# Optimization experiments

Hardware: AMD Instinct MI355X
Metric: run time of the kernel (lower is better)

Reference implementation:

```python
import jax, jax.numpy as jnp
import numpy as np

QI8_MIN, QI8_MAX = -128.0, 127.0   # torch.qint8 iinfo
QU8_MIN, QU8_MAX = 0.0, 255.0      # torch.quint8 iinfo


def _assym_scale_offset(v, qmin, qmax):
    # mirrors get_tensor_assym_scale_offset: scale=(max-min)/(qmax-qmin), offset=qmin - min/scale
    vmin = v.min()
    vmax = v.max()
    scale = (vmax - vmin) / (qmax - qmin)
    offset = qmin - vmin / scale
    return scale, offset


def _fake_quant(v, scale, zp, qmin, qmax):
    # torch.quantize_per_tensor: q = clamp(round(v/scale + zp), qmin, qmax); dequant = (q - zp)*scale
    q = jnp.clip(jnp.round(v / scale + zp), qmin, qmax)
    return (q - zp) * scale


def setup_inputs() -> dict:
    key = jax.random.key(0)
    k1, k2, k3 = jax.random.split(key, 3)
    x = jax.random.normal(k1, (8192, 4096), jnp.float32)          # quantized activation input (modeled as float)
    weight = jax.random.normal(k2, (4096, 4096), jnp.float32) * 0.02  # Linear.weight [out, in]
    bias = jax.random.normal(k3, (4096,), jnp.float32) * 0.01
    return {"x": x, "weight": weight, "bias": bias}


def reference(x, weight, bias):
    # --- weight quantization (qint8, per-tensor asymmetric, done at __init__) ---
    w_scale, w_off = _assym_scale_offset(weight, QI8_MIN, QI8_MAX)
    w_zp = jnp.round(w_off)  # torch casts zero_point to int
    w_dq = _fake_quant(weight, w_scale, w_zp, QI8_MIN, QI8_MAX)

    # --- input is a quint8 quantized tensor; model quantize->dequantize ---
    x_scale, x_off = _assym_scale_offset(x, QU8_MIN, QU8_MAX)
    x_zp = jnp.round(x_off)
    x_dq = _fake_quant(x, x_scale, x_zp, QU8_MIN, QU8_MAX)

    # --- calibration pass (not _computed): float Linear on dequantized input ---
    act = x_dq @ weight.T + bias                 # [tokens, out]
    a_scale, a_off = _assym_scale_offset(act, QU8_MIN, QU8_MAX)
    a_zp = jnp.round(a_off)

    # --- qF.linear: int8 GEMM (dequantized form) + bias, requantized to quint8 ---
    out = x_dq @ w_dq.T + bias
    return _fake_quant(out, a_scale, a_zp, QU8_MIN, QU8_MAX)
```

## Files before the change

kernel.cpp:

```cpp
#include <hip/hip_runtime.h>
#include <stdint.h>

#define M_DIM 8192
#define N_DIM 4096
#define K_DIM 4096

typedef __attribute__((ext_vector_type(4))) int i32x4;

__device__ __forceinline__ unsigned fkey(float f) {
  unsigned u = __float_as_uint(f);
  return (u & 0x80000000u) ? ~u : (u | 0x80000000u);
}
__device__ __forceinline__ float finv(unsigned k) {
  return __uint_as_float((k & 0x80000000u) ? (k ^ 0x80000000u) : ~k);
}
__device__ __forceinline__ void async16(const void* g, void* l) {
  __builtin_amdgcn_global_load_lds(
      (const __attribute__((address_space(1))) void*)g,
      (__attribute__((address_space(3))) void*)l, 16, 0, 0);
}

__global__ void minmax_fused(const float* __restrict__ x, const float* __restrict__ w,
                             unsigned* __restrict__ stats) {
  const bool isX = blockIdx.x < 2048;
  const float4* v4 = isX ? (const float4*)x : (const float4*)w;
  const int n4 = isX ? (M_DIM * K_DIM / 4) : (N_DIM * K_DIM / 4);
  const int bid = isX ? blockIdx.x : (blockIdx.x - 2048);
  const int nb = isX ? 2048 : 1024;
  int i0 = bid * blockDim.x + threadIdx.x;
  int stride = nb * blockDim.x;
  float vmin = 3.4e38f, vmax = -3.4e38f;
  for (int i = i0; i < n4; i += stride) {
    float4 t = v4[i];
    vmin = fminf(vmin, fminf(fminf(t.x, t.y), fminf(t.z, t.w)));
    vmax = fmaxf(vmax, fmaxf(fmaxf(t.x, t.y), fmaxf(t.z, t.w)));
  }
  unsigned kmin = fkey(vmin), kmax = ~fkey(vmax);
  #pragma unroll
  for (int off = 32; off; off >>= 1) {
    unsigned t0 = __shfl_down(kmin, (unsigned)off, 64);
    unsigned t1 = __shfl_down(kmax, (unsigned)off, 64);
    kmin = kmin < t0 ? kmin : t0;
    kmax = kmax < t1 ? kmax : t1;
  }
  if ((threadIdx.x & 63) == 0) {
    int base = isX ? 0 : 2;
    atomicMin(&stats[base + 0], kmin);
    atomicMin(&stats[base + 1], kmax);
  }
}

__global__ void quant_fused(const float* __restrict__ x, const float* __restrict__ w,
                            const unsigned* __restrict__ stats,
                            signed char* __restrict__ A8, signed char* __restrict__ B8,
                            signed char* __restrict__ R8,
                            int* __restrict__ rowA, int* __restrict__ colB, int* __restrict__ colR) {
  __shared__ int sr[8];
  const int tid = threadIdx.x;
  const int lane = tid & 63;
  const int wv = tid >> 6;
  if (blockIdx.x < M_DIM) {
    const int row = blockIdx.x;
    const float xmin = finv(stats[0]), xmax = finv(~stats[1]);
    const float xs = (xmax - xmin) / 255.0f;
    const float xzp = rintf(0.0f - xmin / xs);
    const float4* xr = (const float4*)(x + (size_t)row * K_DIM);
    char4* ar = (char4*)(A8 + (size_t)row * K_DIM);
    int s = 0;
    #pragma unroll
    for (int i = 0; i < 4; ++i) {
      int idx = tid + i * 256;
      float4 t = xr[idx];
      int q0 = (int)(fminf(fmaxf(rintf(t.x / xs + xzp), 0.f), 255.f)) - 128;
      int q1 = (int)(fminf(fmaxf(rintf(t.y / xs + xzp), 0.f), 255.f)) - 128;
      int q2 = (int)(fminf(fmaxf(rintf(t.z / xs + xzp), 0.f), 255.f)) - 128;
      int q3 = (int)(fminf(fmaxf(rintf(t.w / xs + xzp), 0.f), 255.f)) - 128;
      char4 c4; c4.x = (signed char)q0; c4.y = (signed char)q1;
      c4.z = (signed char)q2; c4.w = (signed char)q3;
      ar[idx] = c4;
      s += q0 + q1 + q2 + q3;
    }
    #pragma unroll
    for (int off = 32; off; off >>= 1) s += __shfl_down(s, (unsigned)off, 64);
    if (lane == 0) sr[wv] = s;
    __syncthreads();
    if (tid == 0) rowA[row] = sr[0] + sr[1] + sr[2] + sr[3];
  } else {
    const int row = blockIdx.x - M_DIM;
    const float wmin = finv(stats[2]), wmax = finv(~stats[3]);
    const float ws = (wmax - wmin) / 255.0f;
    const float wzp = rintf(-128.0f - wmin / ws);
    const float inv_rs = 126.0f / ws;
    const float4* wr = (const float4*)(w + (size_t)row * K_DIM);
    char4* br = (char4*)(B8 + (size_t)row * K_DIM);
    char4* rr = (char4*)(R8 + (size_t)row * K_DIM);
    int sb = 0, srr = 0;
    #pragma unroll
    for (int i = 0; i < 4; ++i) {
      int idx = tid + i * 256;
      float4 t = wr[idx];
      char4 bq, rq;
      float v, qf; int q, r;
      v = t.x; qf = fminf(fmaxf(rintf(v / ws + wzp), -128.f), 127.f); q = (int)qf;
      r = (int)fminf(fmaxf(rintf((v - ws * (qf - wzp)) * inv_rs), -127.f), 127.f);
      bq.x = (signed char)q; rq.x = (signed char)r; sb += q; srr += r;
      v = t.y; qf = fminf(fmaxf(rintf(v / ws + wzp), -128.f), 127.f); q = (int)qf;
      r = (int)fminf(fmaxf(rintf((v - ws * (qf - wzp)) * inv_rs), -127.f), 127.f);
      bq.y = (signed char)q; rq.y = (signed char)r; sb += q; srr += r;
      v = t.z; qf = fminf(fmaxf(rintf(v / ws + wzp), -128.f), 127.f); q = (int)qf;
      r = (int)fminf(fmaxf(rintf((v - ws * (qf - wzp)) * inv_rs), -127.f), 127.f);
      bq.z = (signed char)q; rq.z = (signed char)r; sb += q; srr += r;
      v = t.w; qf = fminf(fmaxf(rintf(v / ws + wzp), -128.f), 127.f); q = (int)qf;
      r = (int)fminf(fmaxf(rintf((v - ws * (qf - wzp)) * inv_rs), -127.f), 127.f);
      bq.w = (signed char)q; rq.w = (signed char)r; sb += q; srr += r;
      br[idx] = bq; rr[idx] = rq;
    }
    #pragma unroll
    for (int off = 32; off; off >>= 1) {
      sb += __shfl_down(sb, (unsigned)off, 64);
      srr += __shfl_down(srr, (unsigned)off, 64);
    }
    if (lane == 0) { sr[wv] = sb; sr[4 + wv] = srr; }
    __syncthreads();
    if (tid == 0) {
      colB[row] = sr[0] + sr[1] + sr[2] + sr[3];
      colR[row] = sr[4] + sr[5] + sr[6] + sr[7];
    }
  }
}

__global__ __launch_bounds__(512, 4) void gemm_i8(
    const signed char* __restrict__ A8, const signed char* __restrict__ B8,
    const signed char* __restrict__ R8,
    const int* __restrict__ rowA, const int* __restrict__ colB, const int* __restrict__ colR,
    const float* __restrict__ bias, unsigned* __restrict__ stats,
    float* __restrict__ outp) {
  __shared__ __align__(16) signed char sA[2 * 128 * 64];
  __shared__ __align__(16) signed char sB[2 * 128 * 64];
  __shared__ __align__(16) signed char sR[2 * 128 * 64];
  __shared__ unsigned s_red[2];

  const int tid = threadIdx.x;
  const int wave = tid >> 6;
  const int lane = tid & 63;
  const int xcd = blockIdx.x & 7;
  const int s = blockIdx.x >> 3;
  const int bn = xcd * 4 + (s >> 6);
  const int bm = s & 63;
  const int rowBase = bm * 128;
  const int colBase = bn * 128;
  const int wr = wave >> 2;
  const int wc = wave & 3;
  const int laneR = lane & 15;
  const int laneK = (lane >> 4) * 16;

  if (tid == 0) { s_red[0] = 0xFFFFFFFFu; s_red[1] = 0xFFFFFFFFu; }

  i32x4 acc_q[4][2];
  i32x4 acc_r[4][2];
  const i32x4 zero = {0, 0, 0, 0};
  #pragma unroll
  for (int i = 0; i < 4; ++i) { acc_q[i][0] = zero; acc_q[i][1] = zero;
                                acc_r[i][0] = zero; acc_r[i][1] = zero; }

  const signed char* srcA = A8 + (size_t)(rowBase + wave * 16 + laneR) * K_DIM + laneK;
  const signed char* srcB = B8 + (size_t)(colBase + wave * 16 + laneR) * K_DIM + laneK;
  const signed char* srcR = R8 + (size_t)(colBase + wave * 16 + laneR) * K_DIM + laneK;
  signed char* dA = sA + wave * 1024 + lane * 16;
  signed char* dB = sB + wave * 1024 + lane * 16;
  signed char* dR = sR + wave * 1024 + lane * 16;

#define STAGE(b, kt) do {                        \
    async16(srcA + (kt), dA + (b) * 8192);       \
    async16(srcB + (kt), dB + (b) * 8192);       \
    async16(srcR + (kt), dR + (b) * 8192);       \
  } while (0)

#define COMPUTE(b) do {                                                        \
    i32x4 af[4];                                                               \
    _Pragma("unroll")                                                          \
    for (int mi = 0; mi < 4; ++mi)                                             \
      af[mi] = *(const i32x4*)(sA + (b) * 8192 + (wr * 4 + mi) * 1024 + lane * 16); \
    _Pragma("unroll")                                                          \
    for (int ni = 0; ni < 2; ++ni) {                                           \
      const int bo = (b) * 8192 + (wc * 2 + ni) * 1024 + lane * 16;            \
      i32x4 bf = *(const i32x4*)(sB + bo);                                     \
      i32x4 rf = *(const i32x4*)(sR + bo);                                     \
      _Pragma("unroll")                                                        \
      for (int mi = 0; mi < 4; ++mi) {                                         \
        acc_q[mi][ni] = __builtin_amdgcn_mfma_i32_16x16x64_i8(af[mi], bf, acc_q[mi][ni], 0, 0, 0); \
        acc_r[mi][ni] = __builtin_amdgcn_mfma_i32_16x16x64_i8(af[mi], rf, acc_r[mi][ni], 0, 0, 0); \
      }                                                                        \
    }                                                                          \
  } while (0)

  STAGE(0, 0);
  __syncthreads();

  for (int kt = 0; kt < K_DIM - 128; kt += 128) {
    STAGE(1, kt + 64);
    COMPUTE(0);
    __syncthreads();
    STAGE(0, kt + 128);
    COMPUTE(1);
    __syncthreads();
  }
  STAGE(1, K_DIM - 64);
  COMPUTE(0);
  __syncthreads();
  COMPUTE(1);

#undef STAGE
#undef COMPUTE

  const float xmin = finv(stats[0]), xmax = finv(~stats[1]);
  const float xs = (xmax - xmin) / 255.0f;
  const float xzp = rintf(0.0f - xmin / xs);
  const float wmin = finv(stats[2]), wmax = finv(~stats[3]);
  const float ws = (wmax - wmin) / 255.0f;
  const float wzp = rintf(-128.0f - wmin / ws);
  const int c = 128 - (int)xzp;
  const int wzpi = (int)wzp;
  const float sw = xs * ws;
  const float xrs = xs * (ws / 126.0f);
  const int ccK = c * wzpi * K_DIM;
  unsigned kmin = 0xFFFFFFFFu, kmax = 0xFFFFFFFFu;

  int rAv[4][4];
  #pragma unroll
  for (int mi = 0; mi < 4; ++mi) {
    const int row0 = rowBase + wr * 64 + mi * 16 + (lane >> 4) * 4;
    #pragma unroll
    for (int r = 0; r < 4; ++r) rAv[mi][r] = rowA[row0 + r];
  }

  #pragma unroll
  for (int ni = 0; ni < 2; ++ni) {
    const int col = colBase + wc * 32 + ni * 16 + laneR;
    const float bv = bias[col];
    const int base_n = c * colB[col] - ccK;
    const int cR = c * colR[col];
    #pragma unroll
    for (int mi = 0; mi < 4; ++mi) {
      const int row0 = rowBase + wr * 64 + mi * 16 + (lane >> 4) * 4;
      #pragma unroll
      for (int r = 0; r < 4; ++r) {
        const int S = acc_q[mi][ni][r] + base_n - wzpi * rAv[mi][r];
        const float ov = sw * (float)S + bv;
        const int S2 = acc_r[mi][ni][r] + cR;
        const float av = ov + xrs * (float)S2;
        const unsigned k = fkey(av);
        const unsigned kf = ~k;
        kmin = kmin < k ? kmin : k;
        kmax = kmax < kf ? kmax : kf;
        outp[(size_t)(row0 + r) * N_DIM + col] = ov;
      }
    }
  }

  #pragma unroll
  for (int off = 32; off; off >>= 1) {
    unsigned t0 = __shfl_down(kmin, (unsigned)off, 64);
    unsigned t1 = __shfl_down(kmax, (unsigned)off, 64);
    kmin = kmin < t0 ? kmin : t0;
    kmax = kmax < t1 ? kmax : t1;
  }
  __syncthreads();
  if (lane == 0) { atomicMin(&s_red[0], kmin); atomicMin(&s_red[1], kmax); }
  __syncthreads();
  if (tid == 0) { atomicMin(&stats[4], s_red[0]); atomicMin(&stats[5], s_red[1]); }
}

__global__ void requant_kernel(float* __restrict__ out, const unsigned* __restrict__ stats, int n4) {
  const float amin = finv(stats[4]), amax = finv(~stats[5]);
  const float as = (amax - amin) / 255.0f;
  const float azp = rintf(0.0f - amin / as);
  float4* o4 = (float4*)out;
  int i0 = blockIdx.x * blockDim.x + threadIdx.x;
  int stride = gridDim.x * blockDim.x;
  for (int i = i0; i < n4; i += stride) {
    float4 t = o4[i];
    t.x = (fminf(fmaxf(rintf(t.x / as + azp), 0.f), 255.f) - azp) * as;
    t.y = (fminf(fmaxf(rintf(t.y / as + azp), 0.f), 255.f) - azp) * as;
    t.z = (fminf(fmaxf(rintf(t.z / as + azp), 0.f), 255.f) - azp) * as;
    t.w = (fminf(fmaxf(rintf(t.w / as + azp), 0.f), 255.f) - azp) * as;
    o4[i] = t;
  }
}

extern "C" void kernel_launch(void* const* d_in, const int* in_sizes, int n_in,
                              void* d_out, int out_size, void* d_ws, size_t ws_size,
                              hipStream_t stream) {
  const float* x = (const float*)d_in[0];
  const float* w = (const float*)d_in[1];
  const float* bias = (const float*)d_in[2];
  float* out = (float*)d_out;

  unsigned* stats = (unsigned*)d_ws;
  signed char* A8 = (signed char*)d_ws + 256;
  signed char* B8 = A8 + (size_t)M_DIM * K_DIM;
  signed char* R8 = B8 + (size_t)N_DIM * K_DIM;
  int* rowA = (int*)(R8 + (size_t)N_DIM * K_DIM);
  int* colB = rowA + M_DIM;
  int* colR = colB + N_DIM;

  hipMemsetAsync(stats, 0xFF, 24, stream);
  minmax_fused<<<3072, 256, 0, stream>>>(x, w, stats);
  quant_fused<<<M_DIM + N_DIM, 256, 0, stream>>>(x, w, stats, A8, B8, R8, rowA, colB, colR);
  gemm_i8<<<(M_DIM / 128) * (N_DIM / 128), 512, 0, stream>>>(A8, B8, R8, rowA, colB, colR, bias, stats, out);
  requant_kernel<<<2048, 256, 0, stream>>>(out, stats, M_DIM * N_DIM / 4);
}
```

Baseline: 980.6 us.

## Triple-buffer int8 GEMM LDS staging with vmcnt-gated barriers and MFMA priority

Moves the int8 GEMM main loop from double to triple LDS buffering with rotating offsets. Each step waits with a partial vmcnt instead of a full __syncthreads, so one 64-wide k-tile load stays in flight while the block computes. It also preloads B/R fragments before the MFMA block and raises wave priority around the MFMAs. LDS use per block grows from 48KB to 72KB, which may cut occupancy below the 4 blocks per CU targeted by the launch bounds.

```diff
diff --git a/kernel.cpp b/kernel.cpp
--- a/kernel.cpp
+++ b/kernel.cpp
@@ -135,9 +135,9 @@
     const int* __restrict__ rowA, const int* __restrict__ colB, const int* __restrict__ colR,
     const float* __restrict__ bias, unsigned* __restrict__ stats,
     float* __restrict__ outp) {
-  __shared__ __align__(16) signed char sA[2 * 128 * 64];
-  __shared__ __align__(16) signed char sB[2 * 128 * 64];
-  __shared__ __align__(16) signed char sR[2 * 128 * 64];
+  __shared__ __align__(16) signed char sA[3 * 128 * 64];
+  __shared__ __align__(16) signed char sB[3 * 128 * 64];
+  __shared__ __align__(16) signed char sR[3 * 128 * 64];
   __shared__ unsigned s_red[2];
 
   const int tid = threadIdx.x;
@@ -170,45 +170,55 @@
   signed char* dB = sB + wave * 1024 + lane * 16;
   signed char* dR = sR + wave * 1024 + lane * 16;
 
-#define STAGE(b, kt) do {                        \
-    async16(srcA + (kt), dA + (b) * 8192);       \
-    async16(srcB + (kt), dB + (b) * 8192);       \
-    async16(srcR + (kt), dR + (b) * 8192);       \
+#define STAGE(off, kt) do {                      \
+    async16(srcA + (kt), dA + (off));            \
+    async16(srcB + (kt), dB + (off));            \
+    async16(srcR + (kt), dR + (off));            \
   } while (0)
 
-#define COMPUTE(b) do {                                                        \
+#define COMPUTE(off) do {                                                      \
     i32x4 af[4];                                                               \
     _Pragma("unroll")                                                          \
     for (int mi = 0; mi < 4; ++mi)                                             \
-      af[mi] = *(const i32x4*)(sA + (b) * 8192 + (wr * 4 + mi) * 1024 + lane * 16); \
+      af[mi] = *(const i32x4*)(sA + (off) + (wr * 4 + mi) * 1024 + lane * 16); \
+    i32x4 bf[2], rf[2];                                                        \
     _Pragma("unroll")                                                          \
     for (int ni = 0; ni < 2; ++ni) {                                           \
-      const int bo = (b) * 8192 + (wc * 2 + ni) * 1024 + lane * 16;            \
-      i32x4 bf = *(const i32x4*)(sB + bo);                                     \
-      i32x4 rf = *(const i32x4*)(sR + bo);                                     \
+      const int bo = (off) + (wc * 2 + ni) * 1024 + lane * 16;                 \
+      bf[ni] = *(const i32x4*)(sB + bo);                                       \
+      rf[ni] = *(const i32x4*)(sR + bo);                                       \
+    }                                                                          \
+    __builtin_amdgcn_s_setprio(1);                                             \
+    _Pragma("unroll")                                                          \
+    for (int ni = 0; ni < 2; ++ni) {                                           \
       _Pragma("unroll")                                                        \
       for (int mi = 0; mi < 4; ++mi) {                                         \
-        acc_q[mi][ni] = __builtin_amdgcn_mfma_i32_16x16x64_i8(af[mi], bf, acc_q[mi][ni], 0, 0, 0); \
-        acc_r[mi][ni] = __builtin_amdgcn_mfma_i32_16x16x64_i8(af[mi], rf, acc_r[mi][ni], 0, 0, 0); \
+        acc_q[mi][ni] = __builtin_amdgcn_mfma_i32_16x16x64_i8(af[mi], bf[ni], acc_q[mi][ni], 0, 0, 0); \
+        acc_r[mi][ni] = __builtin_amdgcn_mfma_i32_16x16x64_i8(af[mi], rf[ni], acc_r[mi][ni], 0, 0, 0); \
       }                                                                        \
     }                                                                          \
+    __builtin_amdgcn_s_setprio(0);                                             \
   } while (0)
 
   STAGE(0, 0);
-  __syncthreads();
-
-  for (int kt = 0; kt < K_DIM - 128; kt += 128) {
-    STAGE(1, kt + 64);
-    COMPUTE(0);
-    __syncthreads();
-    STAGE(0, kt + 128);
-    COMPUTE(1);
-    __syncthreads();
-  }
-  STAGE(1, K_DIM - 64);
-  COMPUTE(0);
-  __syncthreads();
-  COMPUTE(1);
+  STAGE(8192, 64);
+
+  int o0 = 0, o1 = 8192, o2 = 16384;
+
+  for (int t = 0; t < 62; ++t) {
+    asm volatile("s_waitcnt vmcnt(3)" ::: "memory");
+    __builtin_amdgcn_s_barrier();
+    STAGE(o2, (t + 2) * 64);
+    COMPUTE(o0);
+    int tmp = o0; o0 = o1; o1 = o2; o2 = tmp;
+  }
+  asm volatile("s_waitcnt vmcnt(3)" ::: "memory");
+  __builtin_amdgcn_s_barrier();
+  COMPUTE(o0);
+  { int tmp = o0; o0 = o1; o1 = o2; o2 = tmp; }
+  asm volatile("s_waitcnt vmcnt(0)" ::: "memory");
+  __builtin_amdgcn_s_barrier();
+  COMPUTE(o0);
 
 #undef STAGE
 #undef COMPUTE
```

Result: no change. 965.2 us (-1.6%).
